# Kernel optimization log

Measured on AMD Instinct MI355X. Metric: run time of the kernel, lower is better.

The kernel has to match this reference:

```python
import jax, jax.numpy as jnp
import numpy as np

B, H, S, E = 1024, 64, 1, 512


def setup_inputs() -> dict:
    key = jax.random.key(0)
    k1, k2, k3, k4, k5 = jax.random.split(key, 5)
    return {
        "others1": jax.random.normal(k1, (B, H, S, E), dtype=jnp.float32),
        "others2": jax.random.normal(k2, (B, H, S, E), dtype=jnp.float32),
        "others3": jax.random.normal(k3, (B, H, S, E), dtype=jnp.float32),
        "main": jax.random.normal(k4, (B, H, S, E), dtype=jnp.float32),
        "W": jax.random.normal(k5, (E, E), dtype=jnp.float32) * 0.02,
    }


def reference(others1, others2, others3, main, W):
    # mean over the 'other' modalities, then drop the seq dim (squeeze(2))
    mean = (others1 + others2 + others3) / 3.0  # (B,H,1,E)
    m = mean[:, :, 0, :]   # (B,H,E)
    q = main[:, :, 0, :]   # (B,H,E)
    # score = mean @ W @ main^T  -> (B,H,H)
    score = jnp.einsum('bhe,ef,bgf->bhg', m, W, q)
    attn = jax.nn.softmax(score, axis=-1)          # (B,H,H)
    context = jnp.einsum('bhg,bge->bhe', attn, q)  # (B,H,E)
    return context, attn
```

## Files before the change

### kernel.cpp

```cpp
#include <hip/hip_runtime.h>
#include <hip/hip_bf16.h>

typedef _Float16 half4_t __attribute__((ext_vector_type(4)));
typedef _Float16 half8_t __attribute__((ext_vector_type(8)));
typedef float    float4_t __attribute__((ext_vector_type(4)));

#define MFMA32(a, b, c) __builtin_amdgcn_mfma_f32_16x16x32_f16((a), (b), (c), 0, 0, 0)

constexpr int  Bb  = 1024;
constexpr long CTX = (long)Bb * 64 * 512;
constexpr int  SVP = 520;
constexpr int  SQP = 40;
constexpr int  QTP = 72;

__global__ void w_pack(const float* __restrict__ W, _Float16* __restrict__ W2) {
    const int t = blockIdx.x * 256 + threadIdx.x;
    const int lane = t & 63, grp = t >> 6;
    const int E = grp >> 4, c = grp & 15;
    const int r16 = lane & 15, q = lane >> 4;
    const float* src = W + (long)(E * 16 + r16) * 512 + c * 32 + q * 8;
    float4_t x = *(const float4_t*)(src);
    float4_t y = *(const float4_t*)(src + 4);
    half8_t h;
    h[0]=(_Float16)x[0]; h[1]=(_Float16)x[1]; h[2]=(_Float16)x[2]; h[3]=(_Float16)x[3];
    h[4]=(_Float16)y[0]; h[5]=(_Float16)y[1]; h[6]=(_Float16)y[2]; h[7]=(_Float16)y[3];
    *(half8_t*)(W2 + (long)t * 8) = h;
}

__global__ __launch_bounds__(512, 4)
void ovo_score(const float* __restrict__ o1, const float* __restrict__ o2,
               const float* __restrict__ o3, const float* __restrict__ qm,
               const _Float16* __restrict__ W2, float* __restrict__ out)
{
    __shared__ __align__(16) _Float16 sV[64 * SVP];
    __shared__ __align__(16) _Float16 sQc[2][64 * SQP];

    const int t = threadIdx.x, lane = t & 63, w = t >> 6;
    const int r16 = lane & 15, q = lane >> 4;
    const long base = (long)blockIdx.x * 64 * 512;
    const float4_t zf4 = {0.f, 0.f, 0.f, 0.f};

    const int sg = t >> 3, sf4 = t & 7;
    const float* qsrc = qm + base + (long)sg * 512 + sf4 * 4;

    float4_t qA, qB;
    auto qcommit = [&](int buf, const float4_t& v) {
        half4_t h;
        h[0]=(_Float16)v[0]; h[1]=(_Float16)v[1]; h[2]=(_Float16)v[2]; h[3]=(_Float16)v[3];
        *(half4_t*)(&sQc[buf][sg * SQP + sf4 * 4]) = h;
    };

    float4_t vacc[4][4];
    #pragma unroll
    for (int i = 0; i < 4; ++i)
        #pragma unroll
        for (int j = 0; j < 4; ++j) vacc[i][j] = zf4;

    auto vcompute = [&](int c, int buf) {
        half8_t Bq[4];
        #pragma unroll
        for (int gt = 0; gt < 4; ++gt)
            Bq[gt] = *(const half8_t*)(&sQc[buf][(gt * 16 + r16) * SQP + q * 8]);
        #pragma unroll
        for (int et = 0; et < 4; ++et) {
            const int E = w * 4 + et;
            half8_t A = *(const half8_t*)(W2 + (long)(E * 16 + c) * 512 + lane * 8);
            #pragma unroll
            for (int gt = 0; gt < 4; ++gt)
                vacc[et][gt] = MFMA32(A, Bq[gt], vacc[et][gt]);
        }
    };

    qA = *(const float4_t*)(qsrc + 0);
    qcommit(0, qA);
    __syncthreads();
    #pragma unroll
    for (int cc = 0; cc < 16; cc += 2) {
        qB = *(const float4_t*)(qsrc + (cc + 1) * 32);
        vcompute(cc, 0);
        qcommit(1, qB);
        __syncthreads();
        if (cc + 2 < 16) qA = *(const float4_t*)(qsrc + (cc + 2) * 32);
        vcompute(cc + 1, 1);
        if (cc + 2 < 16) qcommit(0, qA);
        __syncthreads();
    }

    #pragma unroll
    for (int et = 0; et < 4; ++et) {
        const int e0 = w * 64 + et * 16 + q * 4;
        #pragma unroll
        for (int gt = 0; gt < 4; ++gt)
            #pragma unroll
            for (int r = 0; r < 4; ++r)
                sV[(gt * 16 + r16) * SVP + e0 + r] = (_Float16)vacc[et][gt][r];
    }
    __syncthreads();

    const int ht = w & 3, eh = w >> 2;
    const long abase = base + (long)(ht * 16 + r16) * 512 + eh * 256 + q * 8;
    const int esV = eh * 256 + q * 8;

    float4_t sacc[4];
    #pragma unroll
    for (int i = 0; i < 4; ++i) sacc[i] = zf4;

    float4_t a1A, b1A, a2A, b2A, a3A, b3A;
    float4_t a1B, b1B, a2B, b2B, a3B, b3B;

    #define SLOAD(S, c) do { \
        const long o_ = abase + (c) * 32; \
        a1##S = *(const float4_t*)(o1 + o_); b1##S = *(const float4_t*)(o1 + o_ + 4); \
        a2##S = *(const float4_t*)(o2 + o_); b2##S = *(const float4_t*)(o2 + o_ + 4); \
        a3##S = *(const float4_t*)(o3 + o_); b3##S = *(const float4_t*)(o3 + o_ + 4); \
    } while (0)

    #define SCOMP(S, c) do { \
        float4_t m0 = (a1##S + a2##S + a3##S) * (1.0f / 3.0f); \
        float4_t m1 = (b1##S + b2##S + b3##S) * (1.0f / 3.0f); \
        half8_t af; \
        af[0]=(_Float16)m0[0]; af[1]=(_Float16)m0[1]; af[2]=(_Float16)m0[2]; af[3]=(_Float16)m0[3]; \
        af[4]=(_Float16)m1[0]; af[5]=(_Float16)m1[1]; af[6]=(_Float16)m1[2]; af[7]=(_Float16)m1[3]; \
        _Pragma("unroll") \
        for (int gt = 0; gt < 4; ++gt) { \
            half8_t bf = *(const half8_t*)(&sV[(gt * 16 + r16) * SVP + esV + (c) * 32]); \
            sacc[gt] = MFMA32(af, bf, sacc[gt]); \
        } \
    } while (0)

    SLOAD(A, 0);
    #pragma unroll
    for (int cc = 0; cc < 8; cc += 2) {
        SLOAD(B, cc + 1);
        SCOMP(A, cc);
        if (cc + 2 < 8) SLOAD(A, cc + 2);
        SCOMP(B, cc + 1);
    }

    __syncthreads();
    float* part = reinterpret_cast<float*>(sV);
    if (w >= 4) {
        #pragma unroll
        for (int gt = 0; gt < 4; ++gt)
            *(float4_t*)(&part[(((w - 4) * 4 + gt) * 64 + lane) * 4]) = sacc[gt];
    }
    __syncthreads();
    if (w < 4) {
        #pragma unroll
        for (int gt = 0; gt < 4; ++gt)
            sacc[gt] += *(const float4_t*)(&part[((w * 4 + gt) * 64 + lane) * 4]);
        #pragma unroll
        for (int r = 0; r < 4; ++r) {
            float mx = fmaxf(fmaxf(sacc[0][r], sacc[1][r]), fmaxf(sacc[2][r], sacc[3][r]));
            mx = fmaxf(mx, __shfl_xor(mx, 1));
            mx = fmaxf(mx, __shfl_xor(mx, 2));
            mx = fmaxf(mx, __shfl_xor(mx, 4));
            mx = fmaxf(mx, __shfl_xor(mx, 8));
            float p0 = __expf(sacc[0][r] - mx), p1 = __expf(sacc[1][r] - mx);
            float p2 = __expf(sacc[2][r] - mx), p3 = __expf(sacc[3][r] - mx);
            float s = p0 + p1 + p2 + p3;
            s += __shfl_xor(s, 1); s += __shfl_xor(s, 2);
            s += __shfl_xor(s, 4); s += __shfl_xor(s, 8);
            const float inv = 1.0f / s;
            float* arow = out + CTX + ((long)blockIdx.x * 64 + w * 16 + q * 4 + r) * 64;
            arow[ 0 + r16] = p0 * inv;
            arow[16 + r16] = p1 * inv;
            arow[32 + r16] = p2 * inv;
            arow[48 + r16] = p3 * inv;
        }
    }
}

__global__ __launch_bounds__(256, 4)
void ovo_ctx(const float* __restrict__ qm, const float* __restrict__ out_attn,
             float* __restrict__ out)
{
    __shared__ __align__(16) _Float16 qT[2][64 * QTP];

    const int t = threadIdx.x, lane = t & 63, w = t >> 6;
    const int r16 = lane & 15, q = lane >> 4;
    const long b = blockIdx.x;
    const long base = b * 64 * 512;
    const float4_t zf4 = {0.f, 0.f, 0.f, 0.f};

    const float* ap = out_attn + (b * 64 + w * 16 + r16) * 64 + q * 8;
    half8_t pA0, pA1;
    {
        float4_t x = *(const float4_t*)(ap + 0),  y = *(const float4_t*)(ap + 4);
        pA0[0]=(_Float16)x[0]; pA0[1]=(_Float16)x[1]; pA0[2]=(_Float16)x[2]; pA0[3]=(_Float16)x[3];
        pA0[4]=(_Float16)y[0]; pA0[5]=(_Float16)y[1]; pA0[6]=(_Float16)y[2]; pA0[7]=(_Float16)y[3];
        float4_t z = *(const float4_t*)(ap + 32), u = *(const float4_t*)(ap + 36);
        pA1[0]=(_Float16)z[0]; pA1[1]=(_Float16)z[1]; pA1[2]=(_Float16)z[2]; pA1[3]=(_Float16)z[3];
        pA1[4]=(_Float16)u[0]; pA1[5]=(_Float16)u[1]; pA1[6]=(_Float16)u[2]; pA1[7]=(_Float16)u[3];
    }

    const int sg = t & 63, se = (t >> 6) * 16;
    const float* qsrc = qm + base + (long)sg * 512 + se;
    float4_t rA[4], rB[4];

    #define QLOAD(R, c) do { \
        _Pragma("unroll") \
        for (int i = 0; i < 4; ++i) R[i] = *(const float4_t*)(qsrc + (c) * 64 + i * 4); \
    } while (0)
    #define QCOMMIT(R, buf) do { \
        _Pragma("unroll") \
        for (int i = 0; i < 4; ++i) \
            _Pragma("unroll") \
            for (int jj = 0; jj < 4; ++jj) \
                qT[buf][(se + i * 4 + jj) * QTP + sg] = (_Float16)R[i][jj]; \
    } while (0)

    #define BCOMP(c, buf) do { \
        _Pragma("unroll") \
        for (int et = 0; et < 4; ++et) { \
            half8_t b0 = *(const half8_t*)(&qT[buf][(et * 16 + r16) * QTP + q * 8]); \
            half8_t b1 = *(const half8_t*)(&qT[buf][(et * 16 + r16) * QTP + 32 + q * 8]); \
            float4_t acc = MFMA32(pA0, b0, zf4); \
            acc = MFMA32(pA1, b1, acc); \
            _Pragma("unroll") \
            for (int rr = 0; rr < 4; ++rr) \
                out[(b * 64 + w * 16 + q * 4 + rr) * 512 + (c) * 64 + et * 16 + r16] = acc[rr]; \
        } \
    } while (0)

    QLOAD(rA, 0);
    QCOMMIT(rA, 0);
    __syncthreads();
    #pragma unroll
    for (int cc = 0; cc < 8; cc += 2) {
        QLOAD(rB, cc + 1);
        BCOMP(cc, 0);
        QCOMMIT(rB, 1);
        __syncthreads();
        if (cc + 2 < 8) QLOAD(rA, cc + 2);
        BCOMP(cc + 1, 1);
        if (cc + 2 < 8) QCOMMIT(rA, 0);
        __syncthreads();
    }
}

extern "C" void kernel_launch(void* const* d_in, const int* in_sizes, int n_in,
                              void* d_out, int out_size, void* d_ws, size_t ws_size,
                              hipStream_t stream) {
    const float* o1 = (const float*)d_in[0];
    const float* o2 = (const float*)d_in[1];
    const float* o3 = (const float*)d_in[2];
    const float* qm = (const float*)d_in[3];
    const float* W  = (const float*)d_in[4];
    float* out = (float*)d_out;
    _Float16* W2 = (_Float16*)d_ws;

    w_pack<<<dim3(128), dim3(256), 0, stream>>>(W, W2);
    ovo_score<<<dim3(Bb), dim3(512), 0, stream>>>(o1, o2, o3, qm, W2, out);
    ovo_ctx<<<dim3(Bb), dim3(256), 0, stream>>>(qm, out + CTX, out);
}
```

Measured before the change: 218.4 us.

## Stage full Q tile in LDS once and reuse buffer for V

Replaces the double-buffered, chunk-by-chunk staging of the main tensor with a single up-front load of the whole 64x512 Q tile into LDS as fp16. This removes the per-chunk barriers. The V = Q·W MFMA operand order is swapped so Q is the A operand. The result is written back into the same LDS buffer in a transposed store pattern, which drops the separate sV allocation and lowers shared-memory use. The cost is losing the overlap of global Q loads with the first MFMA chunks, and the new scattered fp16 stores may cause bank conflicts.

```diff
diff --git a/kernel.cpp b/kernel.cpp
--- a/kernel.cpp
+++ b/kernel.cpp
@@ -9,8 +9,7 @@
 
 constexpr int  Bb  = 1024;
 constexpr long CTX = (long)Bb * 64 * 512;
-constexpr int  SVP = 520;
-constexpr int  SQP = 40;
+constexpr int  SQP = 520;
 constexpr int  QTP = 72;
 
 __global__ void w_pack(const float* __restrict__ W, _Float16* __restrict__ W2) {
@@ -32,23 +31,27 @@
                const float* __restrict__ o3, const float* __restrict__ qm,
                const _Float16* __restrict__ W2, float* __restrict__ out)
 {
-    __shared__ __align__(16) _Float16 sV[64 * SVP];
-    __shared__ __align__(16) _Float16 sQc[2][64 * SQP];
+    __shared__ __align__(16) _Float16 sQ[64 * SQP];
 
     const int t = threadIdx.x, lane = t & 63, w = t >> 6;
     const int r16 = lane & 15, q = lane >> 4;
     const long base = (long)blockIdx.x * 64 * 512;
     const float4_t zf4 = {0.f, 0.f, 0.f, 0.f};
 
-    const int sg = t >> 3, sf4 = t & 7;
-    const float* qsrc = qm + base + (long)sg * 512 + sf4 * 4;
-
-    float4_t qA, qB;
-    auto qcommit = [&](int buf, const float4_t& v) {
-        half4_t h;
-        h[0]=(_Float16)v[0]; h[1]=(_Float16)v[1]; h[2]=(_Float16)v[2]; h[3]=(_Float16)v[3];
-        *(half4_t*)(&sQc[buf][sg * SQP + sf4 * 4]) = h;
-    };
+    {
+        const int srow = t >> 3;
+        const int sf   = (t & 7) * 4;
+        const float* qsrc = qm + base + (long)srow * 512 + sf;
+        _Float16*    qdst = &sQ[srow * SQP + sf];
+        #pragma unroll
+        for (int k = 0; k < 16; ++k) {
+            float4_t v = *(const float4_t*)(qsrc + k * 32);
+            half4_t h;
+            h[0]=(_Float16)v[0]; h[1]=(_Float16)v[1]; h[2]=(_Float16)v[2]; h[3]=(_Float16)v[3];
+            *(half4_t*)(qdst + k * 32) = h;
+        }
+    }
+    __syncthreads();
 
     float4_t vacc[4][4];
     #pragma unroll
@@ -56,45 +59,31 @@
         #pragma unroll
         for (int j = 0; j < 4; ++j) vacc[i][j] = zf4;
 
-    auto vcompute = [&](int c, int buf) {
-        half8_t Bq[4];
-        #pragma unroll
-        for (int gt = 0; gt < 4; ++gt)
-            Bq[gt] = *(const half8_t*)(&sQc[buf][(gt * 16 + r16) * SQP + q * 8]);
-        #pragma unroll
-        for (int et = 0; et < 4; ++et) {
-            const int E = w * 4 + et;
-            half8_t A = *(const half8_t*)(W2 + (long)(E * 16 + c) * 512 + lane * 8);
+    #pragma unroll
+    for (int c = 0; c < 16; ++c) {
+        half8_t Aq[4], Bw[4];
+        #pragma unroll
+        for (int gt = 0; gt < 4; ++gt)
+            Aq[gt] = *(const half8_t*)(&sQ[(gt * 16 + r16) * SQP + c * 32 + q * 8]);
+        #pragma unroll
+        for (int et = 0; et < 4; ++et)
+            Bw[et] = *(const half8_t*)(W2 + (long)((w * 4 + et) * 16 + c) * 512 + lane * 8);
+        #pragma unroll
+        for (int gt = 0; gt < 4; ++gt)
             #pragma unroll
-            for (int gt = 0; gt < 4; ++gt)
-                vacc[et][gt] = MFMA32(A, Bq[gt], vacc[et][gt]);
-        }
-    };
-
-    qA = *(const float4_t*)(qsrc + 0);
-    qcommit(0, qA);
-    __syncthreads();
-    #pragma unroll
-    for (int cc = 0; cc < 16; cc += 2) {
-        qB = *(const float4_t*)(qsrc + (cc + 1) * 32);
-        vcompute(cc, 0);
-        qcommit(1, qB);
-        __syncthreads();
-        if (cc + 2 < 16) qA = *(const float4_t*)(qsrc + (cc + 2) * 32);
-        vcompute(cc + 1, 1);
-        if (cc + 2 < 16) qcommit(0, qA);
-        __syncthreads();
-    }
-
-    #pragma unroll
-    for (int et = 0; et < 4; ++et) {
-        const int e0 = w * 64 + et * 16 + q * 4;
-        #pragma unroll
-        for (int gt = 0; gt < 4; ++gt)
+            for (int et = 0; et < 4; ++et)
+                vacc[gt][et] = MFMA32(Aq[gt], Bw[et], vacc[gt][et]);
+    }
+
+    __syncthreads();
+    #pragma unroll
+    for (int gt = 0; gt < 4; ++gt)
+        #pragma unroll
+        for (int et = 0; et < 4; ++et)
             #pragma unroll
             for (int r = 0; r < 4; ++r)
-                sV[(gt * 16 + r16) * SVP + e0 + r] = (_Float16)vacc[et][gt][r];
-    }
+                sQ[(gt * 16 + q * 4 + r) * SQP + w * 64 + et * 16 + r16] =
+                    (_Float16)vacc[gt][et][r];
     __syncthreads();
 
     const int ht = w & 3, eh = w >> 2;
@@ -123,7 +112,7 @@
         af[4]=(_Float16)m1[0]; af[5]=(_Float16)m1[1]; af[6]=(_Float16)m1[2]; af[7]=(_Float16)m1[3]; \
         _Pragma("unroll") \
         for (int gt = 0; gt < 4; ++gt) { \
-            half8_t bf = *(const half8_t*)(&sV[(gt * 16 + r16) * SVP + esV + (c) * 32]); \
+            half8_t bf = *(const half8_t*)(&sQ[(gt * 16 + r16) * SQP + esV + (c) * 32]); \
             sacc[gt] = MFMA32(af, bf, sacc[gt]); \
         } \
     } while (0)
@@ -138,7 +127,7 @@
     }
 
     __syncthreads();
-    float* part = reinterpret_cast<float*>(sV);
+    float* part = reinterpret_cast<float*>(sQ);
     if (w >= 4) {
         #pragma unroll
         for (int gt = 0; gt < 4; ++gt)
```

Result: faster. 211.6 us (-3.1%).
